# Optimization experiments

Measured on AMD Instinct MI355X. Metric: run time of the kernel, lower is better.

Reference implementation:

```python
import jax, jax.numpy as jnp
import numpy as np

N, F_DIM, H, K, T = 4096, 256, 256, 3, 5
START, END = 10, 3  # args.len_numerical_features, args.num_class


def setup_inputs() -> dict:
    key = jax.random.key(0)
    ks = jax.random.split(key, 8)
    s = 0.05
    x = jax.random.normal(ks[0], (N, F_DIM), dtype=jnp.float32)
    adj = jax.random.randint(ks[1], (N, N, K), 0, 2, dtype=jnp.int32)
    gnn_w = jax.random.normal(ks[2], (K, F_DIM, H), dtype=jnp.float32) * s
    gnn_b = jnp.zeros((K, H), dtype=jnp.float32)
    w_ih = jax.random.normal(ks[3], (K, 4 * H, H), dtype=jnp.float32) * s
    w_hh = jax.random.normal(ks[4], (K, 4 * H, H), dtype=jnp.float32) * s
    b_ih = jnp.zeros((K, 4 * H), dtype=jnp.float32)
    b_hh = jnp.zeros((K, 4 * H), dtype=jnp.float32)
    fc_w = jax.random.normal(ks[5], (K, F_DIM, H), dtype=jnp.float32) * s
    fc_b = jnp.zeros((K, F_DIM), dtype=jnp.float32)
    return dict(x=x, gnn_w=gnn_w, gnn_b=gnn_b, w_ih=w_ih, w_hh=w_hh,
                b_ih=b_ih, b_hh=b_hh, fc_w=fc_w, fc_b=fc_b, adj=adj)


def _gcn(x, a_bin, w, b):
    # PyG GCNConv: A_hat = A + I (self-loops added on top of existing edges,
    # weight 1), out = D^-1/2 A_hat D^-1/2 (x @ W) + b
    a = a_bin + jnp.eye(N, dtype=x.dtype)
    deg = a.sum(axis=1)
    dinv = jnp.where(deg > 0, jax.lax.rsqrt(deg), 0.0)
    a_norm = dinv[:, None] * a * dinv[None, :]
    return a_norm @ (x @ w) + b


def _lstm_last(xt, w_ih, w_hh, b_ih, b_hh):
    # batch_first LSTM over T identical inputs xt [N,H]; returns h at last step
    def step(carry, _):
        h, c = carry
        g = xt @ w_ih.T + b_ih + h @ w_hh.T + b_hh
        i, f, gg, o = jnp.split(g, 4, axis=-1)  # torch gate order: i, f, g, o
        c = jax.nn.sigmoid(f) * c + jax.nn.sigmoid(i) * jnp.tanh(gg)
        h = jax.nn.sigmoid(o) * jnp.tanh(c)
        return (h, c), None
    zero = jnp.zeros((xt.shape[0], H), dtype=xt.dtype)
    (h, c), _ = jax.lax.scan(step, (zero, zero), None, length=T)
    return h


def _sig_slice(z):
    return z.at[:, START:F_DIM - END].set(jax.nn.sigmoid(z[:, START:F_DIM - END]))


def reference(x, gnn_w, gnn_b, w_ih, w_hh, b_ih, b_hh, fc_w, fc_b, adj):
    deltas, zbars = [], []
    for k in range(K):
        a_bin = (adj[:, :, k] != 0).astype(x.dtype)
        # GCN output is identical across timesteps -> compute once
        gnn_out = _gcn(x, a_bin, gnn_w[k], gnn_b[k])
        h_last = _lstm_last(gnn_out, w_ih[k], w_hh[k], b_ih[k], b_hh[k])
        delta = jnp.tanh(h_last @ fc_w[k].T + fc_b[k])  # [N, F]
        deltas.append(delta)
        zbars.append(_sig_slice(x + delta))
    delta_z = jnp.stack(deltas, -1).mean(-1)
    res_z_bar = jnp.stack(zbars, -1)  # [N, F, K]
    pred_matrix = _sig_slice(x + delta_z)
    return pred_matrix, res_z_bar, adj
```

## Files before the change

### kernel.cpp

```cpp
#include <hip/hip_runtime.h>
#include <stdint.h>

#define NN_ 4096
#define FD 256
#define HD 256
#define KC 3
#define GD 1024
#define SA 40
#define PAG 40

typedef __attribute__((ext_vector_type(4))) unsigned int vu4;
typedef __attribute__((ext_vector_type(4))) int vi4;
typedef __attribute__((ext_vector_type(4))) float vf4;
typedef __attribute__((ext_vector_type(4))) unsigned short vus4;
typedef __attribute__((ext_vector_type(8))) short short8;
typedef __attribute__((ext_vector_type(4))) float f32x4;

__device__ __forceinline__ float b2f(unsigned short u) {
    unsigned int v = ((unsigned int)u) << 16; float f; __builtin_memcpy(&f, &v, 4); return f;
}
__device__ __forceinline__ unsigned short f2b(float x) {
    unsigned int u; __builtin_memcpy(&u, &x, 4);
    u = (u + 0x7FFFu + ((u >> 16) & 1u)) >> 16;
    return (unsigned short)u;
}
__device__ __forceinline__ void cvt8(const float* __restrict__ g, unsigned short* o) {
    vf4 a = *(const vf4*)g, b = *(const vf4*)(g + 4);
    o[0] = f2b(a[0]); o[1] = f2b(a[1]); o[2] = f2b(a[2]); o[3] = f2b(a[3]);
    o[4] = f2b(b[0]); o[5] = f2b(b[1]); o[6] = f2b(b[2]); o[7] = f2b(b[3]);
}
__device__ __forceinline__ float sigm(float v) { return 1.f / (1.f + __expf(-v)); }

__global__ __launch_bounds__(256) void adj_pass(const int* __restrict__ adj,
        float* __restrict__ adj_out, float* __restrict__ dinv) {
    const int i = blockIdx.x, t = threadIdx.x;
    const vi4* src = (const vi4*)(adj + (size_t)i * 12288);
    vf4* dst = (vf4*)(adj_out + (size_t)i * 12288);
    float s0 = 0.f, s1 = 0.f, s2 = 0.f;
#pragma unroll
    for (int it = 0; it < 12; ++it) {
        int idx = it * 256 + t;
        vi4 v = src[idx];
        float c0 = v[0] ? 1.f : 0.f, c1 = v[1] ? 1.f : 0.f;
        float c2 = v[2] ? 1.f : 0.f, c3 = v[3] ? 1.f : 0.f;
        vf4 w; w[0] = c0; w[1] = c1; w[2] = c2; w[3] = c3;
        dst[idx] = w;
        int m0 = (t + it) % 3;
        float a0 = c0 + c3;
        if (m0 == 0)      { s0 += a0; s1 += c1; s2 += c2; }
        else if (m0 == 1) { s1 += a0; s2 += c1; s0 += c2; }
        else              { s2 += a0; s0 += c1; s1 += c2; }
    }
    __shared__ float r0[256], r1[256], r2[256];
    r0[t] = s0; r1[t] = s1; r2[t] = s2;
    __syncthreads();
    for (int off = 128; off > 0; off >>= 1) {
        if (t < off) { r0[t] += r0[t + off]; r1[t] += r1[t + off]; r2[t] += r2[t + off]; }
        __syncthreads();
    }
    if (t == 0) {
        dinv[i]            = 1.f / sqrtf(1.f + r0[0]);
        dinv[NN_ + i]      = 1.f / sqrtf(1.f + r1[0]);
        dinv[2 * NN_ + i]  = 1.f / sqrtf(1.f + r2[0]);
    }
}

__global__ __launch_bounds__(256) void wcvt(const float* __restrict__ wih,
        const float* __restrict__ whh, const float* __restrict__ fcw,
        unsigned short* __restrict__ wb) {
    size_t e = ((size_t)blockIdx.x * 256 + threadIdx.x) * 8;
    const float* src; size_t off;
    if (e < 786432)       { src = wih; off = e; }
    else if (e < 1572864) { src = whh; off = e - 786432; }
    else                  { src = fcw; off = e - 1572864; }
    alignas(16) unsigned short o[8];
    cvt8(src + off, o);
    *(vu4*)(wb + e) = *(vu4*)o;
}

__global__ __launch_bounds__(256) void gemm_xw(const float* __restrict__ x,
        const float* __restrict__ gw, const float* __restrict__ dinv,
        unsigned short* __restrict__ yT) {
    __shared__ __align__(16) unsigned short sA[64 * SA], sB[64 * SA];
    const int bi = blockIdx.x, bj = blockIdx.y, k = blockIdx.z;
    const int t = threadIdx.x, lane = t & 63, wave = t >> 6;
    const int m = lane & 15, q = lane >> 4, ko = q * 8;
    const int h0 = bj * 64;
    f32x4 acc[4] = {};
    const float* A0 = x + (size_t)(bi * 64) * FD;
    const float* B0 = gw + (size_t)k * FD * HD;
    const int r = t >> 2, c8 = (t & 3) << 3;
    const int fB = t >> 3, c8B = (t & 7) << 3;
    for (int k0 = 0; k0 < FD; k0 += 32) {
        alignas(16) unsigned short tA[8], tB[8];
        cvt8(A0 + (size_t)r * FD + k0 + c8, tA);
        *(vu4*)(sA + r * SA + c8) = *(vu4*)tA;
        cvt8(B0 + (size_t)(k0 + fB) * HD + h0 + c8B, tB);
#pragma unroll
        for (int e = 0; e < 8; ++e) sB[(c8B + e) * SA + fB] = tB[e];
        __syncthreads();
        short8 af = *(const short8*)(sA + (wave * 16 + m) * SA + ko);
#pragma unroll
        for (int ct = 0; ct < 4; ++ct) {
            short8 bf = *(const short8*)(sB + (ct * 16 + m) * SA + ko);
            acc[ct] = __builtin_amdgcn_mfma_f32_16x16x32_bf16(af, bf, acc[ct], 0, 0, 0);
        }
        __syncthreads();
    }
    unsigned short* yTk = yT + (size_t)k * HD * NN_;
#pragma unroll
    for (int ct = 0; ct < 4; ++ct)
#pragma unroll
        for (int r2 = 0; r2 < 4; ++r2) {
            int col = h0 + ct * 16 + m;
            int row = bi * 64 + wave * 16 + q * 4 + r2;
            yTk[(size_t)col * NN_ + row] = f2b(acc[ct][r2] * dinv[(size_t)k * NN_ + row]);
        }
}

__global__ __launch_bounds__(256) void gemm_agg(const float* __restrict__ adjf,
        const unsigned short* __restrict__ yT, unsigned short* __restrict__ pbuf) {
    __shared__ __align__(16) unsigned short sA[3][64 * PAG];
    __shared__ __align__(16) unsigned short sB[3][128 * PAG];
    const int bh = blockIdx.x, bi = blockIdx.y, s = blockIdx.z;
    const int t = threadIdx.x, lane = t & 63, wave = t >> 6;
    const int wi = wave & 1, wh = wave >> 1;
    const int m = lane & 15, q = lane >> 4, ko = q * 8;
    const int i0 = bi * 64, h0 = bh * 128, jbase = s * 1024;
    f32x4 acc[3][2][4] = {};
    for (int j0 = 0; j0 < 1024; j0 += 32) {
#pragma unroll
        for (int g = 0; g < 2; ++g) {
            int idx = g * 256 + t, row = idx >> 3, jq = (idx & 7) << 2;
            const float* src = adjf + (size_t)(i0 + row) * 12288 + (size_t)(jbase + j0 + jq) * 3;
            vf4 v0 = *(const vf4*)src, v1 = *(const vf4*)(src + 4), v2 = *(const vf4*)(src + 8);
            float vv[12] = {v0[0],v0[1],v0[2],v0[3],v1[0],v1[1],v1[2],v1[3],v2[0],v2[1],v2[2],v2[3]};
#pragma unroll
            for (int k = 0; k < 3; ++k) {
                vus4 w;
                w[0] = f2b(vv[0 + k]); w[1] = f2b(vv[3 + k]);
                w[2] = f2b(vv[6 + k]); w[3] = f2b(vv[9 + k]);
                *(vus4*)(&sA[k][row * PAG + jq]) = w;
            }
        }
#pragma unroll
        for (int it = 0; it < 6; ++it) {
            int e = it * 256 + t, k = e >> 9, r = (e & 511) >> 2, c = (e & 3) << 3;
            *(vu4*)(&sB[k][r * PAG + c]) =
                *(const vu4*)(yT + (size_t)(k * 256 + h0 + r) * 4096 + jbase + j0 + c);
        }
        __syncthreads();
        short8 aF[3][2];
#pragma unroll
        for (int k = 0; k < 3; ++k)
#pragma unroll
            for (int rt = 0; rt < 2; ++rt)
                aF[k][rt] = *(const short8*)(&sA[k][(wi * 32 + rt * 16 + m) * PAG + ko]);
#pragma unroll
        for (int k = 0; k < 3; ++k)
#pragma unroll
            for (int ct = 0; ct < 4; ++ct) {
                short8 bF = *(const short8*)(&sB[k][(wh * 64 + ct * 16 + m) * PAG + ko]);
#pragma unroll
                for (int rt = 0; rt < 2; ++rt)
                    acc[k][rt][ct] = __builtin_amdgcn_mfma_f32_16x16x32_bf16(aF[k][rt], bF, acc[k][rt][ct], 0, 0, 0);
            }
        __syncthreads();
    }
    const int addself = (s == (i0 >> 10));
#pragma unroll
    for (int k = 0; k < 3; ++k)
#pragma unroll
        for (int rt = 0; rt < 2; ++rt)
#pragma unroll
            for (int ct = 0; ct < 4; ++ct)
#pragma unroll
                for (int r2 = 0; r2 < 4; ++r2) {
                    int row = i0 + wi * 32 + rt * 16 + q * 4 + r2;
                    int col = h0 + wh * 64 + ct * 16 + m;
                    float v = acc[k][rt][ct][r2];
                    if (addself) v += b2f(yT[((size_t)k * 256 + col) * 4096 + row]);
                    pbuf[(((size_t)s * 3 + k) * 4096 + row) * 256 + col] = f2b(v);
                }
}

__global__ __launch_bounds__(256) void agg_reduce(const unsigned short* __restrict__ pbuf,
        const float* __restrict__ dinv, const float* __restrict__ gnnb,
        unsigned short* __restrict__ xt) {
    size_t e8 = ((size_t)blockIdx.x * 256 + threadIdx.x) * 8;
    int k = (int)(e8 >> 20);
    int i = (int)((e8 >> 8) & 4095);
    int h = (int)(e8 & 255);
    float di = dinv[k * NN_ + i];
    const size_t KIH = (size_t)KC * NN_ * HD;
    alignas(16) unsigned short p0[8], p1[8], p2[8], p3[8], o[8];
    *(vu4*)p0 = *(const vu4*)(pbuf + 0 * KIH + e8);
    *(vu4*)p1 = *(const vu4*)(pbuf + 1 * KIH + e8);
    *(vu4*)p2 = *(const vu4*)(pbuf + 2 * KIH + e8);
    *(vu4*)p3 = *(const vu4*)(pbuf + 3 * KIH + e8);
#pragma unroll
    for (int e = 0; e < 8; ++e) {
        float v = b2f(p0[e]) + b2f(p1[e]) + b2f(p2[e]) + b2f(p3[e]);
        o[e] = f2b(di * v + gnnb[k * HD + h + e]);
    }
    *(vu4*)(xt + e8) = *(vu4*)o;
}

__global__ __launch_bounds__(256) void gemm_nt_ep(const unsigned short* __restrict__ A,
        const unsigned short* __restrict__ W, const float* __restrict__ b1,
        const float* __restrict__ b2, unsigned short* __restrict__ outp,
        int COLS, int do_tanh) {
    __shared__ __align__(16) unsigned short sA[64 * SA], sB[64 * SA];
    const int bg = blockIdx.x, bn = blockIdx.y, k = blockIdx.z;
    const int t = threadIdx.x, lane = t & 63, wave = t >> 6;
    const int m = lane & 15, q = lane >> 4, ko = q * 8;
    f32x4 acc[4] = {};
    const unsigned short* A0 = A + ((size_t)k * NN_ + bn * 64) * HD;
    const unsigned short* W0 = W + ((size_t)k * COLS + bg * 64) * HD;
    const int r = t >> 2, c8 = (t & 3) << 3;
    for (int k0 = 0; k0 < HD; k0 += 32) {
        *(vu4*)(sA + r * SA + c8) = *(const vu4*)(A0 + (size_t)r * HD + k0 + c8);
        *(vu4*)(sB + r * SA + c8) = *(const vu4*)(W0 + (size_t)r * HD + k0 + c8);
        __syncthreads();
        short8 af = *(const short8*)(sA + (wave * 16 + m) * SA + ko);
#pragma unroll
        for (int ct = 0; ct < 4; ++ct) {
            short8 bf = *(const short8*)(sB + (ct * 16 + m) * SA + ko);
            acc[ct] = __builtin_amdgcn_mfma_f32_16x16x32_bf16(af, bf, acc[ct], 0, 0, 0);
        }
        __syncthreads();
    }
#pragma unroll
    for (int ct = 0; ct < 4; ++ct)
#pragma unroll
        for (int r2 = 0; r2 < 4; ++r2) {
            int col = bg * 64 + ct * 16 + m;
            int row = bn * 64 + wave * 16 + q * 4 + r2;
            float v = acc[ct][r2];
            if (b1) v += b1[(size_t)k * COLS + col];
            if (b2) v += b2[(size_t)k * COLS + col];
            if (do_tanh) v = tanhf(v);
            outp[((size_t)k * NN_ + row) * COLS + col] = f2b(v);
        }
}

__global__ __launch_bounds__(256) void lstm_step(const unsigned short* __restrict__ hprev,
        const unsigned short* __restrict__ whhb, const unsigned short* __restrict__ gateX,
        unsigned short* __restrict__ cbuf, unsigned short* __restrict__ hnext, int first) {
    __shared__ __align__(16) unsigned short sA[64 * SA];
    __shared__ __align__(16) unsigned short sB[4][64 * SA];
    const int t = threadIdx.x, lane = t & 63, wave = t >> 6;
    const int m = lane & 15, q = lane >> 4, ko = q * 8;
    const int bc = blockIdx.x, bn = blockIdx.y, k = blockIdx.z;
    const int c0 = bc * 64;
    f32x4 acc[4][4] = {};
    if (!first) {
        const unsigned short* A0 = hprev + ((size_t)k * NN_ + bn * 64) * HD;
        const unsigned short* W0 = whhb + (size_t)k * GD * HD;
        const int r = t >> 2, c8 = (t & 3) << 3;
        for (int k0 = 0; k0 < HD; k0 += 32) {
            *(vu4*)(sA + r * SA + c8) = *(const vu4*)(A0 + (size_t)r * HD + k0 + c8);
#pragma unroll
            for (int gt = 0; gt < 4; ++gt)
                *(vu4*)(&sB[gt][r * SA + c8]) =
                    *(const vu4*)(W0 + (size_t)(gt * 256 + c0 + r) * HD + k0 + c8);
            __syncthreads();
            short8 af = *(const short8*)(sA + (wave * 16 + m) * SA + ko);
#pragma unroll
            for (int gt = 0; gt < 4; ++gt)
#pragma unroll
                for (int ct = 0; ct < 4; ++ct) {
                    short8 bf = *(const short8*)(&sB[gt][(ct * 16 + m) * SA + ko]);
                    acc[gt][ct] = __builtin_amdgcn_mfma_f32_16x16x32_bf16(af, bf, acc[gt][ct], 0, 0, 0);
                }
            __syncthreads();
        }
    }
    const unsigned short* gX = gateX + ((size_t)k * NN_ + bn * 64) * GD;
    unsigned short* crow = cbuf + ((size_t)k * NN_ + bn * 64) * HD;
    unsigned short* hrow = hnext + ((size_t)k * NN_ + bn * 64) * HD;
#pragma unroll
    for (int ct = 0; ct < 4; ++ct)
#pragma unroll
        for (int r2 = 0; r2 < 4; ++r2) {
            int row = wave * 16 + q * 4 + r2;
            int col = c0 + ct * 16 + m;
            float iv = acc[0][ct][r2] + b2f(gX[(size_t)row * GD + 0 * 256 + col]);
            float fv = acc[1][ct][r2] + b2f(gX[(size_t)row * GD + 1 * 256 + col]);
            float gv = acc[2][ct][r2] + b2f(gX[(size_t)row * GD + 2 * 256 + col]);
            float ov = acc[3][ct][r2] + b2f(gX[(size_t)row * GD + 3 * 256 + col]);
            float cold = first ? 0.f : b2f(crow[(size_t)row * HD + col]);
            float cn = sigm(fv) * cold + sigm(iv) * tanhf(gv);
            float hn = sigm(ov) * tanhf(cn);
            crow[(size_t)row * HD + col] = f2b(cn);
            hrow[(size_t)row * HD + col] = f2b(hn);
        }
}

__global__ __launch_bounds__(256) void final_ep(const float* __restrict__ x,
        const unsigned short* __restrict__ delta, float* __restrict__ pred,
        float* __restrict__ res) {
    int idx = blockIdx.x * 256 + threadIdx.x;
    size_t base = (size_t)idx * 8;
    int f0 = (int)(base & 255);
    alignas(16) unsigned short d0[8], d1[8], d2[8];
    alignas(16) float pr[8], rs[24];
    vf4 xa = *(const vf4*)(x + base), xb = *(const vf4*)(x + base + 4);
    float xs[8] = { xa[0], xa[1], xa[2], xa[3], xb[0], xb[1], xb[2], xb[3] };
    *(vu4*)d0 = *(const vu4*)(delta + base);
    *(vu4*)d1 = *(const vu4*)(delta + (size_t)NN_ * FD + base);
    *(vu4*)d2 = *(const vu4*)(delta + 2 * (size_t)NN_ * FD + base);
#pragma unroll
    for (int e = 0; e < 8; ++e) {
        int f = f0 + e;
        bool sg = (f >= 10) && (f < 253);
        float xf = xs[e];
        float da = b2f(d0[e]), db = b2f(d1[e]), dc = b2f(d2[e]);
        float dm = (da + db + dc) * (1.f / 3.f);
        float p = xf + dm; if (sg) p = sigm(p);
        pr[e] = p;
        float z0 = xf + da; if (sg) z0 = sigm(z0);
        float z1 = xf + db; if (sg) z1 = sigm(z1);
        float z2 = xf + dc; if (sg) z2 = sigm(z2);
        rs[e * 3 + 0] = z0; rs[e * 3 + 1] = z1; rs[e * 3 + 2] = z2;
    }
    *(vf4*)(pred + base)     = *(vf4*)pr;
    *(vf4*)(pred + base + 4) = *(vf4*)(pr + 4);
    size_t rb = base * 3;
#pragma unroll
    for (int v = 0; v < 6; ++v)
        *(vf4*)(res + rb + v * 4) = *(vf4*)(rs + v * 4);
}

extern "C" void kernel_launch(void* const* d_in, const int* in_sizes, int n_in,
                              void* d_out, int out_size, void* d_ws, size_t ws_size,
                              hipStream_t stream) {
    const float* x    = (const float*)d_in[0];
    const float* gnnw = (const float*)d_in[1];
    const float* gnnb = (const float*)d_in[2];
    const float* wih  = (const float*)d_in[3];
    const float* whh  = (const float*)d_in[4];
    const float* bih  = (const float*)d_in[5];
    const float* bhh  = (const float*)d_in[6];
    const float* fcw  = (const float*)d_in[7];
    const float* fcb  = (const float*)d_in[8];
    const int*   adj  = (const int*)d_in[9];

    float* out = (float*)d_out;
    float* out_pred = out;
    float* out_res  = out + (size_t)NN_ * FD;
    float* out_adj  = out + (size_t)NN_ * FD * 4;

    char* ws = (char*)d_ws;
    float*          dinv  = (float*)ws;
    unsigned short* R1    = (unsigned short*)(ws + 49152);
    unsigned short* R2    = (unsigned short*)(ws + 6340608);
    unsigned short* wb    = (unsigned short*)(ws + 12632064);
    unsigned short* pbuf  = (unsigned short*)(ws + 16171008);
    unsigned short* gateX = pbuf;
    unsigned short* hA    = (unsigned short*)(ws + 41336832);
    unsigned short* cbuf  = (unsigned short*)(ws + 47628288);
    const unsigned short* wihb = wb;
    const unsigned short* whhb = wb + 786432;
    const unsigned short* fcwb = wb + 1572864;
    (void)ws_size; (void)in_sizes; (void)n_in; (void)out_size;

    wcvt<<<dim3(864), 256, 0, stream>>>(wih, whh, fcw, wb);
    adj_pass<<<dim3(4096), 256, 0, stream>>>(adj, out_adj, dinv);
    gemm_xw<<<dim3(64, 4, 3), 256, 0, stream>>>(x, gnnw, dinv, R1 );
    gemm_agg<<<dim3(2, 64, 4), 256, 0, stream>>>(out_adj, R1 , pbuf);
    agg_reduce<<<dim3(1536), 256, 0, stream>>>(pbuf, dinv, gnnb, R2 );
    gemm_nt_ep<<<dim3(16, 64, 3), 256, 0, stream>>>(R2 , wihb, bih, bhh, gateX, GD, 0);
    for (int tstep = 0; tstep < 5; ++tstep) {
        unsigned short* hp = (tstep & 1) ? R1 : hA;
        unsigned short* hn = (tstep & 1) ? hA : R1;
        lstm_step<<<dim3(4, 64, 3), 256, 0, stream>>>(hp, whhb, gateX, cbuf, hn, tstep == 0 ? 1 : 0);
    }
    gemm_nt_ep<<<dim3(4, 64, 3), 256, 0, stream>>>(R1 , fcwb, fcb, nullptr, R2 , FD, 1);
    final_ep<<<dim3(512), 256, 0, stream>>>(x, R2 , out_pred, out_res);
}
```

Measured before the change: 687.0 us.

## Fuse LSTM timesteps into one kernel and precompute bf16 per-relation adjacency

The five per-timestep LSTM launches become one persistent kernel per 32-row tile. It keeps h in shared memory and c in registers across steps, and gate pre-activations are stored gate-interleaved so each element needs one vector load. The adjacency pass now also writes a bf16 per-relation copy, so the aggregation GEMM loads A tiles directly instead of converting fp32 on every tile. In exchange, W_hh is re-streamed for every small row tile, only 384 blocks are launched, and an extra 100MB of bf16 adjacency is written.

```diff
diff --git a/kernel.cpp b/kernel.cpp
--- a/kernel.cpp
+++ b/kernel.cpp
@@ -8,6 +8,8 @@
 #define GD 1024
 #define SA 40
 #define PAG 40
+#define HP 264
+#define BP 40
 
 typedef __attribute__((ext_vector_type(4))) unsigned int vu4;
 typedef __attribute__((ext_vector_type(4))) int vi4;
@@ -32,24 +34,36 @@
 __device__ __forceinline__ float sigm(float v) { return 1.f / (1.f + __expf(-v)); }
 
 __global__ __launch_bounds__(256) void adj_pass(const int* __restrict__ adj,
-        float* __restrict__ adj_out, float* __restrict__ dinv) {
+        float* __restrict__ adj_out, unsigned short* __restrict__ abk,
+        float* __restrict__ dinv) {
     const int i = blockIdx.x, t = threadIdx.x;
-    const vi4* src = (const vi4*)(adj + (size_t)i * 12288);
-    vf4* dst = (vf4*)(adj_out + (size_t)i * 12288);
+    const int* src = adj + (size_t)i * 12288;
+    float* dstf = adj_out + (size_t)i * 12288;
     float s0 = 0.f, s1 = 0.f, s2 = 0.f;
 #pragma unroll
-    for (int it = 0; it < 12; ++it) {
-        int idx = it * 256 + t;
-        vi4 v = src[idx];
-        float c0 = v[0] ? 1.f : 0.f, c1 = v[1] ? 1.f : 0.f;
-        float c2 = v[2] ? 1.f : 0.f, c3 = v[3] ? 1.f : 0.f;
-        vf4 w; w[0] = c0; w[1] = c1; w[2] = c2; w[3] = c3;
-        dst[idx] = w;
-        int m0 = (t + it) % 3;
-        float a0 = c0 + c3;
-        if (m0 == 0)      { s0 += a0; s1 += c1; s2 += c2; }
-        else if (m0 == 1) { s1 += a0; s2 += c1; s0 += c2; }
-        else              { s2 += a0; s0 += c1; s1 += c2; }
+    for (int it = 0; it < 4; ++it) {
+        int jq = (it * 256 + t) * 4;
+        vi4 a = *(const vi4*)(src + jq * 3);
+        vi4 b = *(const vi4*)(src + jq * 3 + 4);
+        vi4 c = *(const vi4*)(src + jq * 3 + 8);
+        int vv[12] = {a[0],a[1],a[2],a[3],b[0],b[1],b[2],b[3],c[0],c[1],c[2],c[3]};
+        float ff[12];
+#pragma unroll
+        for (int e = 0; e < 12; ++e) ff[e] = vv[e] ? 1.f : 0.f;
+        vf4 w0 = {ff[0],ff[1],ff[2],ff[3]}, w1 = {ff[4],ff[5],ff[6],ff[7]}, w2 = {ff[8],ff[9],ff[10],ff[11]};
+        *(vf4*)(dstf + jq * 3) = w0; *(vf4*)(dstf + jq * 3 + 4) = w1; *(vf4*)(dstf + jq * 3 + 8) = w2;
+#pragma unroll
+        for (int k = 0; k < 3; ++k) {
+            vus4 w;
+            w[0] = vv[k]     ? (unsigned short)0x3F80 : (unsigned short)0;
+            w[1] = vv[3 + k] ? (unsigned short)0x3F80 : (unsigned short)0;
+            w[2] = vv[6 + k] ? (unsigned short)0x3F80 : (unsigned short)0;
+            w[3] = vv[9 + k] ? (unsigned short)0x3F80 : (unsigned short)0;
+            *(vus4*)(abk + ((size_t)(k * NN_ + i)) * NN_ + jq) = w;
+        }
+        s0 += ff[0] + ff[3] + ff[6] + ff[9];
+        s1 += ff[1] + ff[4] + ff[7] + ff[10];
+        s2 += ff[2] + ff[5] + ff[8] + ff[11];
     }
     __shared__ float r0[256], r1[256], r2[256];
     r0[t] = s0; r1[t] = s1; r2[t] = s2;
@@ -118,7 +132,7 @@
         }
 }
 
-__global__ __launch_bounds__(256) void gemm_agg(const float* __restrict__ adjf,
+__global__ __launch_bounds__(256) void gemm_agg(const unsigned short* __restrict__ abk,
         const unsigned short* __restrict__ yT, unsigned short* __restrict__ pbuf) {
     __shared__ __align__(16) unsigned short sA[3][64 * PAG];
     __shared__ __align__(16) unsigned short sB[3][128 * PAG];
@@ -128,21 +142,13 @@
     const int m = lane & 15, q = lane >> 4, ko = q * 8;
     const int i0 = bi * 64, h0 = bh * 128, jbase = s * 1024;
     f32x4 acc[3][2][4] = {};
+    const int rA = t >> 2, jg = (t & 3) << 3;
+    const int rB = (t & 511) >> 2;
     for (int j0 = 0; j0 < 1024; j0 += 32) {
 #pragma unroll
-        for (int g = 0; g < 2; ++g) {
-            int idx = g * 256 + t, row = idx >> 3, jq = (idx & 7) << 2;
-            const float* src = adjf + (size_t)(i0 + row) * 12288 + (size_t)(jbase + j0 + jq) * 3;
-            vf4 v0 = *(const vf4*)src, v1 = *(const vf4*)(src + 4), v2 = *(const vf4*)(src + 8);
-            float vv[12] = {v0[0],v0[1],v0[2],v0[3],v1[0],v1[1],v1[2],v1[3],v2[0],v2[1],v2[2],v2[3]};
-#pragma unroll
-            for (int k = 0; k < 3; ++k) {
-                vus4 w;
-                w[0] = f2b(vv[0 + k]); w[1] = f2b(vv[3 + k]);
-                w[2] = f2b(vv[6 + k]); w[3] = f2b(vv[9 + k]);
-                *(vus4*)(&sA[k][row * PAG + jq]) = w;
-            }
-        }
+        for (int p = 0; p < 3; ++p)
+            *(vu4*)(&sA[p][rA * PAG + jg]) =
+                *(const vu4*)(abk + ((size_t)(p * NN_ + i0 + rA)) * NN_ + jbase + j0 + jg);
 #pragma unroll
         for (int it = 0; it < 6; ++it) {
             int e = it * 256 + t, k = e >> 9, r = (e & 511) >> 2, c = (e & 3) << 3;
@@ -167,6 +173,7 @@
             }
         __syncthreads();
     }
+    (void)rB;
     const int addself = (s == (i0 >> 10));
 #pragma unroll
     for (int k = 0; k < 3; ++k)
@@ -209,7 +216,7 @@
 __global__ __launch_bounds__(256) void gemm_nt_ep(const unsigned short* __restrict__ A,
         const unsigned short* __restrict__ W, const float* __restrict__ b1,
         const float* __restrict__ b2, unsigned short* __restrict__ outp,
-        int COLS, int do_tanh) {
+        int COLS, int do_tanh, int gate_ilv) {
     __shared__ __align__(16) unsigned short sA[64 * SA], sB[64 * SA];
     const int bg = blockIdx.x, bn = blockIdx.y, k = blockIdx.z;
     const int t = threadIdx.x, lane = t & 63, wave = t >> 6;
@@ -240,61 +247,85 @@
             if (b1) v += b1[(size_t)k * COLS + col];
             if (b2) v += b2[(size_t)k * COLS + col];
             if (do_tanh) v = tanhf(v);
-            outp[((size_t)k * NN_ + row) * COLS + col] = f2b(v);
-        }
-}
-
-__global__ __launch_bounds__(256) void lstm_step(const unsigned short* __restrict__ hprev,
-        const unsigned short* __restrict__ whhb, const unsigned short* __restrict__ gateX,
-        unsigned short* __restrict__ cbuf, unsigned short* __restrict__ hnext, int first) {
-    __shared__ __align__(16) unsigned short sA[64 * SA];
-    __shared__ __align__(16) unsigned short sB[4][64 * SA];
-    const int t = threadIdx.x, lane = t & 63, wave = t >> 6;
+            if (gate_ilv) {
+                int gate = col >> 8, ch = col & 255;
+                outp[(((size_t)k * NN_ + row) * 256 + ch) * 4 + gate] = f2b(v);
+            } else {
+                outp[((size_t)k * NN_ + row) * COLS + col] = f2b(v);
+            }
+        }
+}
+
+__global__ __launch_bounds__(256) void lstm_fused(const unsigned short* __restrict__ gX2,
+        const unsigned short* __restrict__ whhb, unsigned short* __restrict__ hout) {
+    __shared__ __align__(16) unsigned short sH[32 * HP];
+    __shared__ __align__(16) unsigned short sB[512 * BP];
+    const int t = threadIdx.x, lane = t & 63, wh = t >> 6;
     const int m = lane & 15, q = lane >> 4, ko = q * 8;
-    const int bc = blockIdx.x, bn = blockIdx.y, k = blockIdx.z;
-    const int c0 = bc * 64;
-    f32x4 acc[4][4] = {};
-    if (!first) {
-        const unsigned short* A0 = hprev + ((size_t)k * NN_ + bn * 64) * HD;
-        const unsigned short* W0 = whhb + (size_t)k * GD * HD;
-        const int r = t >> 2, c8 = (t & 3) << 3;
-        for (int k0 = 0; k0 < HD; k0 += 32) {
-            *(vu4*)(sA + r * SA + c8) = *(const vu4*)(A0 + (size_t)r * HD + k0 + c8);
-#pragma unroll
-            for (int gt = 0; gt < 4; ++gt)
-                *(vu4*)(&sB[gt][r * SA + c8]) =
-                    *(const vu4*)(W0 + (size_t)(gt * 256 + c0 + r) * HD + k0 + c8);
-            __syncthreads();
-            short8 af = *(const short8*)(sA + (wave * 16 + m) * SA + ko);
-#pragma unroll
-            for (int gt = 0; gt < 4; ++gt)
-#pragma unroll
-                for (int ct = 0; ct < 4; ++ct) {
-                    short8 bf = *(const short8*)(&sB[gt][(ct * 16 + m) * SA + ko]);
-                    acc[gt][ct] = __builtin_amdgcn_mfma_f32_16x16x32_bf16(af, bf, acc[gt][ct], 0, 0, 0);
+    const int bi = blockIdx.x, k = blockIdx.y;
+    const int n0 = bi * 32;
+    const unsigned short* W0 = whhb + (size_t)k * GD * HD;
+    const unsigned short* gX = gX2 + ((size_t)(k * NN_ + n0)) * 1024;
+    float c[2][4][4] = {};
+    for (int step = 0; step < 5; ++step) {
+        f32x4 acc[2][4][4] = {};
+        if (step > 0) {
+            for (int k0 = 0; k0 < 256; k0 += 32) {
+#pragma unroll
+                for (int hf = 0; hf < 2; ++hf) {
+#pragma unroll
+                    for (int it = 0; it < 8; ++it) {
+                        int e = it * 256 + t, r = e >> 2, c8 = (e & 3) << 3;
+                        int g = r >> 7, ch = hf * 128 + (r & 127);
+                        *(vu4*)(&sB[r * BP + c8]) =
+                            *(const vu4*)(W0 + (size_t)(g * 256 + ch) * 256 + k0 + c8);
+                    }
+                    __syncthreads();
+                    short8 af[2];
+#pragma unroll
+                    for (int rt = 0; rt < 2; ++rt)
+                        af[rt] = *(const short8*)(&sH[(rt * 16 + m) * HP + k0 + ko]);
+#pragma unroll
+                    for (int g = 0; g < 4; ++g)
+#pragma unroll
+                        for (int c2 = 0; c2 < 2; ++c2) {
+                            short8 bf = *(const short8*)(&sB[(g * 128 + wh * 32 + c2 * 16 + m) * BP + ko]);
+                            int cc = hf * 2 + c2;
+#pragma unroll
+                            for (int rt = 0; rt < 2; ++rt)
+                                acc[rt][g][cc] = __builtin_amdgcn_mfma_f32_16x16x32_bf16(af[rt], bf, acc[rt][g][cc], 0, 0, 0);
+                        }
+                    __syncthreads();
                 }
-            __syncthreads();
-        }
-    }
-    const unsigned short* gX = gateX + ((size_t)k * NN_ + bn * 64) * GD;
-    unsigned short* crow = cbuf + ((size_t)k * NN_ + bn * 64) * HD;
-    unsigned short* hrow = hnext + ((size_t)k * NN_ + bn * 64) * HD;
-#pragma unroll
-    for (int ct = 0; ct < 4; ++ct)
-#pragma unroll
-        for (int r2 = 0; r2 < 4; ++r2) {
-            int row = wave * 16 + q * 4 + r2;
-            int col = c0 + ct * 16 + m;
-            float iv = acc[0][ct][r2] + b2f(gX[(size_t)row * GD + 0 * 256 + col]);
-            float fv = acc[1][ct][r2] + b2f(gX[(size_t)row * GD + 1 * 256 + col]);
-            float gv = acc[2][ct][r2] + b2f(gX[(size_t)row * GD + 2 * 256 + col]);
-            float ov = acc[3][ct][r2] + b2f(gX[(size_t)row * GD + 3 * 256 + col]);
-            float cold = first ? 0.f : b2f(crow[(size_t)row * HD + col]);
-            float cn = sigm(fv) * cold + sigm(iv) * tanhf(gv);
-            float hn = sigm(ov) * tanhf(cn);
-            crow[(size_t)row * HD + col] = f2b(cn);
-            hrow[(size_t)row * HD + col] = f2b(hn);
-        }
+            }
+        }
+#pragma unroll
+        for (int rt = 0; rt < 2; ++rt)
+#pragma unroll
+            for (int cc = 0; cc < 4; ++cc) {
+                int hf = cc >> 1, c2 = cc & 1;
+                int col = hf * 128 + wh * 32 + c2 * 16 + m;
+#pragma unroll
+                for (int r2 = 0; r2 < 4; ++r2) {
+                    int row = rt * 16 + q * 4 + r2;
+                    vus4 gv = *(const vus4*)(gX + ((size_t)row * 256 + col) * 4);
+                    float iv = acc[rt][0][cc][r2] + b2f(gv[0]);
+                    float fv = acc[rt][1][cc][r2] + b2f(gv[1]);
+                    float gg = acc[rt][2][cc][r2] + b2f(gv[2]);
+                    float ov = acc[rt][3][cc][r2] + b2f(gv[3]);
+                    float cn = sigm(fv) * c[rt][cc][r2] + sigm(iv) * tanhf(gg);
+                    c[rt][cc][r2] = cn;
+                    sH[row * HP + col] = f2b(sigm(ov) * tanhf(cn));
+                }
+            }
+        __syncthreads();
+    }
+    unsigned short* dst = hout + ((size_t)(k * NN_ + n0)) * 256;
+#pragma unroll
+    for (int it = 0; it < 4; ++it) {
+        int e = it * 256 + t, row = e >> 5, c8 = (e & 31) << 3;
+        *(vu4*)(dst + (size_t)row * 256 + c8) = *(const vu4*)(&sH[row * HP + c8]);
+    }
 }
 
 __global__ __launch_bounds__(256) void final_ep(const float* __restrict__ x,
@@ -357,25 +388,20 @@
     unsigned short* R2    = (unsigned short*)(ws + 6340608);
     unsigned short* wb    = (unsigned short*)(ws + 12632064);
     unsigned short* pbuf  = (unsigned short*)(ws + 16171008);
-    unsigned short* gateX = pbuf;
-    unsigned short* hA    = (unsigned short*)(ws + 41336832);
-    unsigned short* cbuf  = (unsigned short*)(ws + 47628288);
+    unsigned short* gX2   = pbuf;
+    unsigned short* abk   = (unsigned short*)(ws + 41336832);
     const unsigned short* wihb = wb;
     const unsigned short* whhb = wb + 786432;
     const unsigned short* fcwb = wb + 1572864;
     (void)ws_size; (void)in_sizes; (void)n_in; (void)out_size;
 
     wcvt<<<dim3(864), 256, 0, stream>>>(wih, whh, fcw, wb);
-    adj_pass<<<dim3(4096), 256, 0, stream>>>(adj, out_adj, dinv);
+    adj_pass<<<dim3(4096), 256, 0, stream>>>(adj, out_adj, abk, dinv);
     gemm_xw<<<dim3(64, 4, 3), 256, 0, stream>>>(x, gnnw, dinv, R1 );
-    gemm_agg<<<dim3(2, 64, 4), 256, 0, stream>>>(out_adj, R1 , pbuf);
+    gemm_agg<<<dim3(2, 64, 4), 256, 0, stream>>>(abk, R1 , pbuf);
     agg_reduce<<<dim3(1536), 256, 0, stream>>>(pbuf, dinv, gnnb, R2 );
-    gemm_nt_ep<<<dim3(16, 64, 3), 256, 0, stream>>>(R2 , wihb, bih, bhh, gateX, GD, 0);
-    for (int tstep = 0; tstep < 5; ++tstep) {
-        unsigned short* hp = (tstep & 1) ? R1 : hA;
-        unsigned short* hn = (tstep & 1) ? hA : R1;
-        lstm_step<<<dim3(4, 64, 3), 256, 0, stream>>>(hp, whhb, gateX, cbuf, hn, tstep == 0 ? 1 : 0);
-    }
-    gemm_nt_ep<<<dim3(4, 64, 3), 256, 0, stream>>>(R1 , fcwb, fcb, nullptr, R2 , FD, 1);
+    gemm_nt_ep<<<dim3(16, 64, 3), 256, 0, stream>>>(R2 , wihb, bih, bhh, gX2, GD, 0, 1);
+    lstm_fused<<<dim3(128, 3), 256, 0, stream>>>(gX2, whhb, R1 );
+    gemm_nt_ep<<<dim3(4, 64, 3), 256, 0, stream>>>(R1, fcwb, fcb, nullptr, R2 , FD, 1, 0);
     final_ep<<<dim3(512), 256, 0, stream>>>(x, R2 , out_pred, out_res);
 }
```

After: 948.2 us. 38.0% more time.
